# Optimization experiments

Hardware: AMD Instinct MI355X
Metric: run time of the kernel (lower is better)

Reference implementation:

```python
import jax, jax.numpy as jnp
import numpy as np

N_NODES = 50000
N_EDGES = 600000
N_GRAPHS = 1000
IN_DIM = 128   # atom_feat_dim
HID = 128      # emb_dim
NEG_SLOPE = 0.01


def setup_inputs() -> dict:
    key = jax.random.key(0)
    k = jax.random.split(key, 6)
    drug_x = jax.random.normal(k[0], (N_NODES, IN_DIM), dtype=jnp.float32)
    edge_index = jax.random.randint(k[1], (2, N_EDGES), 0, N_NODES, dtype=jnp.int32)
    batch = jnp.sort(jax.random.randint(k[2], (N_NODES,), 0, N_GRAPHS, dtype=jnp.int32))
    # GCNConv parameters (glorot-ish init for weights, zero bias, as in PyG)
    W1 = jax.random.normal(k[3], (IN_DIM, HID), dtype=jnp.float32) * (1.0 / np.sqrt(IN_DIM))
    b1 = jnp.zeros((HID,), dtype=jnp.float32)
    W2 = jax.random.normal(k[4], (HID, HID), dtype=jnp.float32) * (1.0 / np.sqrt(HID))
    b2 = jnp.zeros((HID,), dtype=jnp.float32)
    return {"drug_x": drug_x, "W1": W1, "b1": b1, "W2": W2, "b2": b2,
            "edge_index": edge_index, "batch": batch}


def _gcn_conv(x, W, b, src, dst, n_nodes):
    """PyG GCNConv: lin -> add self-loops -> deg^-1/2 sym norm -> scatter-add -> +bias."""
    h = x @ W  # [N, H]
    ones = jnp.ones(src.shape[0], dtype=h.dtype)
    # degree on the target side, +1 for the self-loop
    deg = jax.ops.segment_sum(ones, dst, num_segments=n_nodes) + 1.0
    dinv = jax.lax.rsqrt(deg)  # [N]
    coef = dinv[src] * dinv[dst]  # [E]
    agg = jax.ops.segment_sum(h[src] * coef[:, None], dst, num_segments=n_nodes)
    # self-loop contribution: dinv[i]*dinv[i]*h[i]
    agg = agg + h * (dinv * dinv)[:, None]
    return agg + b


def _leaky_relu(x):
    return jnp.where(x > 0, x, NEG_SLOPE * x)


def reference(drug_x, W1, b1, W2, b2, edge_index, batch):
    src, dst = edge_index[0], edge_index[1]
    n = drug_x.shape[0]
    h = _leaky_relu(_gcn_conv(drug_x, W1, b1, src, dst, n))  # dropout = identity (eval)
    h = _leaky_relu(_gcn_conv(h, W2, b2, src, dst, n))
    # global_mean_pool over graph ids
    sums = jax.ops.segment_sum(h, batch, num_segments=N_GRAPHS)
    counts = jax.ops.segment_sum(jnp.ones((n,), h.dtype), batch, num_segments=N_GRAPHS)
    return sums / jnp.maximum(counts, 1.0)[:, None]
```

## Files before the change

### kernel.cpp

```cpp
#include <hip/hip_runtime.h>

#define DIM 128
#define NEG_SLOPE 0.01f
#define ELLW 64
#define CPAD 16
#define LDA 136
#define SPLIT 4
#define WPAD 132

typedef short short8 __attribute__((ext_vector_type(8)));
typedef float f32x4 __attribute__((ext_vector_type(4)));

__device__ __forceinline__ unsigned short f2bf(float f) {
    unsigned u = __float_as_uint(f);
    u = u + 0x7FFFu + ((u >> 16) & 1u);
    return (unsigned short)(u >> 16);
}
__device__ __forceinline__ float bf2f(unsigned short s) {
    return __uint_as_float((unsigned)s << 16);
}

__global__ __launch_bounds__(256) void k_fillprep(const int* __restrict__ src,
                                                  const int* __restrict__ dst,
                                                  int* __restrict__ cursorPad,
                                                  int* __restrict__ eSrc,
                                                  const float* __restrict__ W1,
                                                  const float* __restrict__ W2,
                                                  unsigned short* __restrict__ Wt1,
                                                  unsigned short* __restrict__ Wt2,
                                                  int nE) {
    int i = blockIdx.x * 256 + threadIdx.x;
    if (i < nE) {
        int s = src[i], d = dst[i];
        int pos = atomicAdd(&cursorPad[d * CPAD], 1);
        if (pos < ELLW) eSrc[(size_t)d * ELLW + pos] = s;
    }
    if (i < 32768) {
        const float* W = (i < 16384) ? W1 : W2;
        unsigned short* Wt = (i < 16384) ? Wt1 : Wt2;
        int j = i & 16383;
        int k = j >> 7, n = j & 127;
        Wt[n * 128 + k] = f2bf(W[k * 128 + n]);
    }
}

__global__ __launch_bounds__(256) void k_gemm(const float* __restrict__ X,
                                              const unsigned short* __restrict__ Wt,
                                              const int* __restrict__ cursorPad,
                                              unsigned short* __restrict__ Y, int nRows) {
    __shared__ unsigned short sA[64 * LDA];
    const int t = threadIdx.x;
    const int row0 = blockIdx.x * 64;

#pragma unroll
    for (int rep = 0; rep < 8; ++rep) {
        int idx = t + rep * 256;
        int r = idx >> 5, k4 = (idx & 31) * 4;
        int gr = row0 + r;
        float4 v = make_float4(0.f, 0.f, 0.f, 0.f);
        if (gr < nRows) v = *(const float4*)&X[(size_t)gr * 128 + k4];
        ushort4 p;
        p.x = f2bf(v.x); p.y = f2bf(v.y); p.z = f2bf(v.z); p.w = f2bf(v.w);
        *(ushort4*)&sA[r * LDA + k4] = p;
    }
    __syncthreads();

    const int wave = t >> 6, lane = t & 63;
    const int l15 = lane & 15;
    const int koff = (lane >> 4) * 8;
    const int arow = wave * 16 + l15;

    short8 a[4];
#pragma unroll
    for (int ks = 0; ks < 4; ++ks)
        a[ks] = *(const short8*)&sA[arow * LDA + ks * 32 + koff];

    f32x4 acc[8];
#pragma unroll
    for (int c = 0; c < 8; ++c) acc[c] = (f32x4){0.f, 0.f, 0.f, 0.f};
#pragma unroll
    for (int c = 0; c < 8; ++c) {
        const unsigned short* wp = Wt + (size_t)(c * 16 + l15) * 128 + koff;
#pragma unroll
        for (int ks = 0; ks < 4; ++ks) {
            short8 b = *(const short8*)(wp + ks * 32);
            acc[c] = __builtin_amdgcn_mfma_f32_16x16x32_bf16(a[ks], b, acc[c], 0, 0, 0);
        }
    }
    const int orow = row0 + wave * 16 + (lane >> 4) * 4;
#pragma unroll
    for (int r = 0; r < 4; ++r) {
        int gr = orow + r;
        if (gr < nRows) {
            float dv = rsqrtf((float)cursorPad[gr * CPAD] + 1.0f);
#pragma unroll
            for (int c = 0; c < 8; ++c)
                Y[(size_t)gr * 128 + c * 16 + l15] = f2bf(acc[c][r] * dv);
        }
    }
}

#define ACCUM(v)                                         \
    do {                                                 \
        acc[0] += bf2f((v).x & 0xFFFFu);                 \
        acc[1] += __uint_as_float((v).x & 0xFFFF0000u);  \
        acc[2] += bf2f((v).y & 0xFFFFu);                 \
        acc[3] += __uint_as_float((v).y & 0xFFFF0000u);  \
        acc[4] += bf2f((v).z & 0xFFFFu);                 \
        acc[5] += __uint_as_float((v).z & 0xFFFF0000u);  \
        acc[6] += bf2f((v).w & 0xFFFFu);                 \
        acc[7] += __uint_as_float((v).w & 0xFFFF0000u);  \
    } while (0)

__device__ __forceinline__ void gather_body(const uint4* __restrict__ h4,
                                            const int* __restrict__ cursorPad,
                                            const int* __restrict__ eSrc,
                                            const float* __restrict__ bias,
                                            int i, int l, float* acc) {
    const int beg = i * ELLW;
    const int cnt = cursorPad[i * CPAD];
    const int deg = min(cnt, ELLW);
    const int end = beg + deg;
    const float di = rsqrtf((float)cnt + 1.0f);

    {
        uint4 hv = h4[(size_t)i * 16 + l];
        acc[0] = bf2f(hv.x & 0xFFFFu);
        acc[1] = __uint_as_float(hv.x & 0xFFFF0000u);
        acc[2] = bf2f(hv.y & 0xFFFFu);
        acc[3] = __uint_as_float(hv.y & 0xFFFF0000u);
        acc[4] = bf2f(hv.z & 0xFFFFu);
        acc[5] = __uint_as_float(hv.z & 0xFFFF0000u);
        acc[6] = bf2f(hv.w & 0xFFFFu);
        acc[7] = __uint_as_float(hv.w & 0xFFFF0000u);
    }
    int e = beg;
    for (; e + 8 <= end; e += 8) {
        int4 s0 = *(const int4*)&eSrc[e];
        int4 s1 = *(const int4*)&eSrc[e + 4];
        uint4 v[8];
        v[0] = h4[(size_t)s0.x * 16 + l];
        v[1] = h4[(size_t)s0.y * 16 + l];
        v[2] = h4[(size_t)s0.z * 16 + l];
        v[3] = h4[(size_t)s0.w * 16 + l];
        v[4] = h4[(size_t)s1.x * 16 + l];
        v[5] = h4[(size_t)s1.y * 16 + l];
        v[6] = h4[(size_t)s1.z * 16 + l];
        v[7] = h4[(size_t)s1.w * 16 + l];
#pragma unroll
        for (int j = 0; j < 8; ++j) ACCUM(v[j]);
    }
    if (e + 4 <= end) {
        int4 s0 = *(const int4*)&eSrc[e];
        uint4 v[4];
        v[0] = h4[(size_t)s0.x * 16 + l];
        v[1] = h4[(size_t)s0.y * 16 + l];
        v[2] = h4[(size_t)s0.z * 16 + l];
        v[3] = h4[(size_t)s0.w * 16 + l];
#pragma unroll
        for (int j = 0; j < 4; ++j) ACCUM(v[j]);
        e += 4;
    }
    if (e + 2 <= end) {
        int s0 = eSrc[e], s1 = eSrc[e + 1];
        uint4 v0 = h4[(size_t)s0 * 16 + l];
        uint4 v1 = h4[(size_t)s1 * 16 + l];
        ACCUM(v0);
        ACCUM(v1);
        e += 2;
    }
    if (e < end) {
        int s0 = eSrc[e];
        uint4 v0 = h4[(size_t)s0 * 16 + l];
        ACCUM(v0);
    }

    float4 b0 = *(const float4*)&bias[l * 8];
    float4 b1 = *(const float4*)&bias[l * 8 + 4];
    acc[0] = acc[0] * di + b0.x; acc[0] = acc[0] > 0.f ? acc[0] : NEG_SLOPE * acc[0];
    acc[1] = acc[1] * di + b0.y; acc[1] = acc[1] > 0.f ? acc[1] : NEG_SLOPE * acc[1];
    acc[2] = acc[2] * di + b0.z; acc[2] = acc[2] > 0.f ? acc[2] : NEG_SLOPE * acc[2];
    acc[3] = acc[3] * di + b0.w; acc[3] = acc[3] > 0.f ? acc[3] : NEG_SLOPE * acc[3];
    acc[4] = acc[4] * di + b1.x; acc[4] = acc[4] > 0.f ? acc[4] : NEG_SLOPE * acc[4];
    acc[5] = acc[5] * di + b1.y; acc[5] = acc[5] > 0.f ? acc[5] : NEG_SLOPE * acc[5];
    acc[6] = acc[6] * di + b1.z; acc[6] = acc[6] > 0.f ? acc[6] : NEG_SLOPE * acc[6];
    acc[7] = acc[7] * di + b1.w; acc[7] = acc[7] > 0.f ? acc[7] : NEG_SLOPE * acc[7];
}
#undef ACCUM

__global__ __launch_bounds__(256) void k_gg(const uint4* __restrict__ h4in,
                                            const int* __restrict__ cursorPad,
                                            const int* __restrict__ eSrc,
                                            const float* __restrict__ bias,
                                            const unsigned short* __restrict__ Wt,
                                            unsigned short* __restrict__ Y, int nN) {
    __shared__ unsigned short sA[64 * LDA];
    const int t = threadIdx.x;
    const int row0 = blockIdx.x * 64;
    const int lg = t >> 4;
    const int l = t & 15;

#pragma unroll
    for (int p = 0; p < 4; ++p) {
        int r = p * 16 + lg;
        int i = row0 + r;
        float acc[8];
        if (i < nN) {
            gather_body(h4in, cursorPad, eSrc, bias, i, l, acc);
        } else {
#pragma unroll
            for (int j = 0; j < 8; ++j) acc[j] = 0.0f;
        }
        ushort4 p0, p1;
        p0.x = f2bf(acc[0]); p0.y = f2bf(acc[1]); p0.z = f2bf(acc[2]); p0.w = f2bf(acc[3]);
        p1.x = f2bf(acc[4]); p1.y = f2bf(acc[5]); p1.z = f2bf(acc[6]); p1.w = f2bf(acc[7]);
        *(ushort4*)&sA[r * LDA + l * 8] = p0;
        *(ushort4*)&sA[r * LDA + l * 8 + 4] = p1;
    }
    __syncthreads();

    const int wave = t >> 6, lane = t & 63;
    const int l15 = lane & 15;
    const int koff = (lane >> 4) * 8;
    const int arow = wave * 16 + l15;

    short8 a[4];
#pragma unroll
    for (int ks = 0; ks < 4; ++ks)
        a[ks] = *(const short8*)&sA[arow * LDA + ks * 32 + koff];

    f32x4 acc[8];
#pragma unroll
    for (int c = 0; c < 8; ++c) acc[c] = (f32x4){0.f, 0.f, 0.f, 0.f};
#pragma unroll
    for (int c = 0; c < 8; ++c) {
        const unsigned short* wp = Wt + (size_t)(c * 16 + l15) * 128 + koff;
#pragma unroll
        for (int ks = 0; ks < 4; ++ks) {
            short8 b = *(const short8*)(wp + ks * 32);
            acc[c] = __builtin_amdgcn_mfma_f32_16x16x32_bf16(a[ks], b, acc[c], 0, 0, 0);
        }
    }
    const int orow = row0 + wave * 16 + (lane >> 4) * 4;
#pragma unroll
    for (int r = 0; r < 4; ++r) {
        int gr = orow + r;
        if (gr < nN) {
            float dv = rsqrtf((float)cursorPad[gr * CPAD] + 1.0f);
#pragma unroll
            for (int c = 0; c < 8; ++c)
                Y[(size_t)gr * 128 + c * 16 + l15] = f2bf(acc[c][r] * dv);
        }
    }
}

__global__ __launch_bounds__(256) void k_gp(const uint4* __restrict__ h4in,
                                            const int* __restrict__ cursorPad,
                                            const int* __restrict__ eSrc,
                                            const float* __restrict__ bias,
                                            const int* __restrict__ batch,
                                            float* __restrict__ out, int nN, int nG) {
    __shared__ float accW[4 * WPAD];
    __shared__ int bounds[2];
    const int g = blockIdx.x / SPLIT;
    const int part = blockIdx.x % SPLIT;
    const int t = threadIdx.x;
    if (t == 0) {
        int lo = 0, hi = nN;
        while (lo < hi) { int m = (lo + hi) >> 1; if (batch[m] < g) lo = m + 1; else hi = m; }
        bounds[0] = lo;
        hi = nN;
        while (lo < hi) { int m = (lo + hi) >> 1; if (batch[m] < g + 1) lo = m + 1; else hi = m; }
        bounds[1] = lo;
    }
    __syncthreads();
    const int beg = bounds[0], end = bounds[1];
    const int lg = t >> 4, l = t & 15;
    const int wave = t >> 6, lane = t & 63;

    float acc8[8];
#pragma unroll
    for (int j = 0; j < 8; ++j) acc8[j] = 0.0f;

    for (int base = beg + part * 16; base < end; base += SPLIT * 16) {
        int i = base + lg;
        if (i < end) {
            float a[8];
            gather_body(h4in, cursorPad, eSrc, bias, i, l, a);
#pragma unroll
            for (int j = 0; j < 8; ++j) acc8[j] += a[j];
        }
    }
#pragma unroll
    for (int j = 0; j < 8; ++j) {
        acc8[j] += __shfl_down(acc8[j], 32);
        acc8[j] += __shfl_down(acc8[j], 16);
    }
    if (lane < 16) {
        *(float4*)&accW[wave * WPAD + lane * 8] =
            make_float4(acc8[0], acc8[1], acc8[2], acc8[3]);
        *(float4*)&accW[wave * WPAD + lane * 8 + 4] =
            make_float4(acc8[4], acc8[5], acc8[6], acc8[7]);
    }
    __syncthreads();
    if (t < 128) {
        float s = accW[0 * WPAD + t] + accW[1 * WPAD + t] +
                  accW[2 * WPAD + t] + accW[3 * WPAD + t];
        float cnt = (float)(end - beg);
        atomicAdd(&out[(size_t)g * DIM + t], s / fmaxf(cnt, 1.0f));
    }
}

extern "C" void kernel_launch(void* const* d_in, const int* in_sizes, int n_in,
                              void* d_out, int out_size, void* d_ws, size_t ws_size,
                              hipStream_t stream) {
    const float* X  = (const float*)d_in[0];
    const float* W1 = (const float*)d_in[1];
    const float* b1 = (const float*)d_in[2];
    const float* W2 = (const float*)d_in[3];
    const float* b2 = (const float*)d_in[4];
    const int*   ei = (const int*)d_in[5];
    const int*   batch = (const int*)d_in[6];
    float* out = (float*)d_out;

    const int NN = in_sizes[0] / DIM;
    const int NE = in_sizes[5] / 2;
    const int NG = out_size / DIM;

    const int* src = ei;
    const int* dst = ei + NE;

    char* ws = (char*)d_ws;
    size_t o = 0;
    auto alloc = [&](size_t bytes) {
        char* p = ws + o;
        o += (bytes + 1023) & ~(size_t)1023;
        return p;
    };
    int* cursorPad = (int*)alloc((size_t)NN * CPAD * 4);
    unsigned short* Wt1 = (unsigned short*)alloc((size_t)16384 * 2);
    unsigned short* Wt2 = (unsigned short*)alloc((size_t)16384 * 2);
    int*   eSrc    = (int*)alloc((size_t)NN * ELLW * 4);
    unsigned short* bufA = (unsigned short*)alloc((size_t)NN * DIM * 2);
    unsigned short* bufB = (unsigned short*)alloc((size_t)NN * DIM * 2);

    hipMemsetAsync(cursorPad, 0, (size_t)NN * CPAD * 4, stream);
    hipMemsetAsync(out, 0, (size_t)out_size * 4, stream);

    const int B = 256;

    k_fillprep<<<(NE + B - 1) / B, B, 0, stream>>>(src, dst, cursorPad, eSrc,
                                                   W1, W2, Wt1, Wt2, NE);

    int tile_grid = (NN + 63) / 64;

    k_gemm<<<tile_grid, B, 0, stream>>>(X, Wt1, cursorPad, bufA, NN);

    k_gg<<<tile_grid, B, 0, stream>>>((const uint4*)bufA, cursorPad, eSrc, b1,
                                      Wt2, bufB, NN);

    k_gp<<<NG * SPLIT, B, 0, stream>>>((const uint4*)bufB, cursorPad, eSrc, b2,
                                       batch, out, NN, NG);
}
```

Measured before the change: 219.0 us.

## Shrink gather-GEMM tile to 16 rows and precompute graph offsets

The fused gather+GEMM kernel now processes 16 rows per block instead of 64. Each of the four waves computes two 16-column output blocks of the same 16 rows, giving four times as many blocks to raise occupancy and spread the latency-bound gather. Separately, graph segment offsets are computed once in the prep kernel from the sorted batch array, replacing two per-block binary searches and a barrier in the pooling kernel. The cost is that each block now reloads the full W2 from global or cache for only 16 rows of output.

```diff
diff --git a/kernel.cpp b/kernel.cpp
--- a/kernel.cpp
+++ b/kernel.cpp
@@ -22,18 +22,28 @@
 
 __global__ __launch_bounds__(256) void k_fillprep(const int* __restrict__ src,
                                                   const int* __restrict__ dst,
+                                                  const int* __restrict__ batch,
                                                   int* __restrict__ cursorPad,
                                                   int* __restrict__ eSrc,
                                                   const float* __restrict__ W1,
                                                   const float* __restrict__ W2,
                                                   unsigned short* __restrict__ Wt1,
                                                   unsigned short* __restrict__ Wt2,
-                                                  int nE) {
+                                                  int* __restrict__ gOff,
+                                                  int nE, int nN, int nG) {
     int i = blockIdx.x * 256 + threadIdx.x;
     if (i < nE) {
         int s = src[i], d = dst[i];
         int pos = atomicAdd(&cursorPad[d * CPAD], 1);
         if (pos < ELLW) eSrc[(size_t)d * ELLW + pos] = s;
+    }
+    if (i < nN) {
+        int b1 = batch[i];
+        int b0 = (i == 0) ? -1 : batch[i - 1];
+        for (int g = b0 + 1; g <= b1; ++g) gOff[g] = i;
+        if (i == nN - 1) {
+            for (int g = b1 + 1; g <= nG; ++g) gOff[g] = nN;
+        }
     }
     if (i < 32768) {
         const float* W = (i < 16384) ? W1 : W2;
@@ -194,16 +204,14 @@
                                             const float* __restrict__ bias,
                                             const unsigned short* __restrict__ Wt,
                                             unsigned short* __restrict__ Y, int nN) {
-    __shared__ unsigned short sA[64 * LDA];
+    __shared__ unsigned short sA[16 * LDA];
     const int t = threadIdx.x;
-    const int row0 = blockIdx.x * 64;
+    const int row0 = blockIdx.x * 16;
     const int lg = t >> 4;
     const int l = t & 15;
 
-#pragma unroll
-    for (int p = 0; p < 4; ++p) {
-        int r = p * 16 + lg;
-        int i = row0 + r;
+    {
+        int i = row0 + lg;
         float acc[8];
         if (i < nN) {
             gather_body(h4in, cursorPad, eSrc, bias, i, l, acc);
@@ -214,42 +222,42 @@
         ushort4 p0, p1;
         p0.x = f2bf(acc[0]); p0.y = f2bf(acc[1]); p0.z = f2bf(acc[2]); p0.w = f2bf(acc[3]);
         p1.x = f2bf(acc[4]); p1.y = f2bf(acc[5]); p1.z = f2bf(acc[6]); p1.w = f2bf(acc[7]);
-        *(ushort4*)&sA[r * LDA + l * 8] = p0;
-        *(ushort4*)&sA[r * LDA + l * 8 + 4] = p1;
+        *(ushort4*)&sA[lg * LDA + l * 8] = p0;
+        *(ushort4*)&sA[lg * LDA + l * 8 + 4] = p1;
     }
     __syncthreads();
 
     const int wave = t >> 6, lane = t & 63;
     const int l15 = lane & 15;
     const int koff = (lane >> 4) * 8;
-    const int arow = wave * 16 + l15;
 
     short8 a[4];
 #pragma unroll
     for (int ks = 0; ks < 4; ++ks)
-        a[ks] = *(const short8*)&sA[arow * LDA + ks * 32 + koff];
-
-    f32x4 acc[8];
-#pragma unroll
-    for (int c = 0; c < 8; ++c) acc[c] = (f32x4){0.f, 0.f, 0.f, 0.f};
-#pragma unroll
-    for (int c = 0; c < 8; ++c) {
+        a[ks] = *(const short8*)&sA[l15 * LDA + ks * 32 + koff];
+
+    f32x4 acc[2];
+#pragma unroll
+    for (int cb = 0; cb < 2; ++cb) acc[cb] = (f32x4){0.f, 0.f, 0.f, 0.f};
+#pragma unroll
+    for (int cb = 0; cb < 2; ++cb) {
+        const int c = wave * 2 + cb;
         const unsigned short* wp = Wt + (size_t)(c * 16 + l15) * 128 + koff;
 #pragma unroll
         for (int ks = 0; ks < 4; ++ks) {
             short8 b = *(const short8*)(wp + ks * 32);
-            acc[c] = __builtin_amdgcn_mfma_f32_16x16x32_bf16(a[ks], b, acc[c], 0, 0, 0);
-        }
-    }
-    const int orow = row0 + wave * 16 + (lane >> 4) * 4;
+            acc[cb] = __builtin_amdgcn_mfma_f32_16x16x32_bf16(a[ks], b, acc[cb], 0, 0, 0);
+        }
+    }
+    const int orow = row0 + (lane >> 4) * 4;
 #pragma unroll
     for (int r = 0; r < 4; ++r) {
         int gr = orow + r;
         if (gr < nN) {
             float dv = rsqrtf((float)cursorPad[gr * CPAD] + 1.0f);
 #pragma unroll
-            for (int c = 0; c < 8; ++c)
-                Y[(size_t)gr * 128 + c * 16 + l15] = f2bf(acc[c][r] * dv);
+            for (int cb = 0; cb < 2; ++cb)
+                Y[(size_t)gr * 128 + (wave * 2 + cb) * 16 + l15] = f2bf(acc[cb][r] * dv);
         }
     }
 }
@@ -258,23 +266,13 @@
                                             const int* __restrict__ cursorPad,
                                             const int* __restrict__ eSrc,
                                             const float* __restrict__ bias,
-                                            const int* __restrict__ batch,
+                                            const int* __restrict__ gOff,
                                             float* __restrict__ out, int nN, int nG) {
     __shared__ float accW[4 * WPAD];
-    __shared__ int bounds[2];
     const int g = blockIdx.x / SPLIT;
     const int part = blockIdx.x % SPLIT;
     const int t = threadIdx.x;
-    if (t == 0) {
-        int lo = 0, hi = nN;
-        while (lo < hi) { int m = (lo + hi) >> 1; if (batch[m] < g) lo = m + 1; else hi = m; }
-        bounds[0] = lo;
-        hi = nN;
-        while (lo < hi) { int m = (lo + hi) >> 1; if (batch[m] < g + 1) lo = m + 1; else hi = m; }
-        bounds[1] = lo;
-    }
-    __syncthreads();
-    const int beg = bounds[0], end = bounds[1];
+    const int beg = gOff[g], end = gOff[g + 1];
     const int lg = t >> 4, l = t & 15;
     const int wave = t >> 6, lane = t & 63;
 
@@ -338,6 +336,7 @@
         return p;
     };
     int* cursorPad = (int*)alloc((size_t)NN * CPAD * 4);
+    int* gOff      = (int*)alloc((size_t)(NG + 1) * 4);
     unsigned short* Wt1 = (unsigned short*)alloc((size_t)16384 * 2);
     unsigned short* Wt2 = (unsigned short*)alloc((size_t)16384 * 2);
     int*   eSrc    = (int*)alloc((size_t)NN * ELLW * 4);
@@ -349,16 +348,14 @@
 
     const int B = 256;
 
-    k_fillprep<<<(NE + B - 1) / B, B, 0, stream>>>(src, dst, cursorPad, eSrc,
-                                                   W1, W2, Wt1, Wt2, NE);
-
-    int tile_grid = (NN + 63) / 64;
-
-    k_gemm<<<tile_grid, B, 0, stream>>>(X, Wt1, cursorPad, bufA, NN);
-
-    k_gg<<<tile_grid, B, 0, stream>>>((const uint4*)bufA, cursorPad, eSrc, b1,
-                                      Wt2, bufB, NN);
+    k_fillprep<<<(NE + B - 1) / B, B, 0, stream>>>(src, dst, batch, cursorPad, eSrc,
+                                                   W1, W2, Wt1, Wt2, gOff, NE, NN, NG);
+
+    k_gemm<<<(NN + 63) / 64, B, 0, stream>>>(X, Wt1, cursorPad, bufA, NN);
+
+    k_gg<<<(NN + 15) / 16, B, 0, stream>>>((const uint4*)bufA, cursorPad, eSrc, b1,
+                                           Wt2, bufB, NN);
 
     k_gp<<<NG * SPLIT, B, 0, stream>>>((const uint4*)bufB, cursorPad, eSrc, b2,
-                                       batch, out, NN, NG);
-}
+                                       gOff, out, NN, NG);
+}
```

Result: faster. 201.7 us, median of 2 (-7.9%).
